# Kernel optimization log

Measured on AMD Instinct MI355X. Metric: run time of the kernel, lower is better.

The kernel has to match this reference:

```python
import jax, jax.numpy as jnp
import numpy as np

B, T, H = 8192, 24, 1024


def setup_inputs() -> dict:
    key = jax.random.key(0)
    ks = jax.random.split(key, 16)
    n = lambda k, shp, s=1.0: (jax.random.normal(k, shp, dtype=jnp.float32) * s)
    return {
        "x": n(ks[0], (B, T, 1)),
        "h1_0": n(ks[1], (B, H), 0.02),
        "c1_0": n(ks[2], (B, H), 0.02),
        "h2_0": n(ks[3], (B, H), 0.02),
        "c2_0": n(ks[4], (B, H), 0.02),
        "W_ih1": n(ks[5], (4 * H, 1), 0.05),
        "W_hh1": n(ks[6], (4 * H, H), 0.02),
        "b_ih1": n(ks[7], (4 * H,), 0.02),
        "b_hh1": n(ks[8], (4 * H,), 0.02),
        "W_ih2": n(ks[9], (4 * H, H), 0.02),
        "W_hh2": n(ks[10], (4 * H, H), 0.02),
        "b_ih2": n(ks[11], (4 * H,), 0.02),
        "b_hh2": n(ks[12], (4 * H,), 0.02),
        "W_out": n(ks[13], (2, H), 0.02),
        "b_out": jnp.array([0.2, -0.2], dtype=jnp.float32),
    }


def _lstm_cell(x_t, h, c, W_ih, W_hh, b_ih, b_hh):
    # PyTorch LSTMCell: gates ordered (i, f, g, o)
    gates = x_t @ W_ih.T + b_ih + h @ W_hh.T + b_hh  # [B, 4H]
    i, f, g, o = jnp.split(gates, 4, axis=-1)
    c_new = jax.nn.sigmoid(f) * c + jax.nn.sigmoid(i) * jnp.tanh(g)
    h_new = jax.nn.sigmoid(o) * jnp.tanh(c_new)
    return h_new, c_new


def reference(x, h1_0, c1_0, h2_0, c2_0,
              W_ih1, W_hh1, b_ih1, b_hh1,
              W_ih2, W_hh2, b_ih2, b_hh2,
              W_out, b_out):
    xs = jnp.transpose(x, (1, 0, 2))  # [T, B, 1]

    def step(carry, x_t):
        h1, c1, h2, c2 = carry
        h1, c1 = _lstm_cell(x_t, h1, c1, W_ih1, W_hh1, b_ih1, b_hh1)
        h2, c2 = _lstm_cell(h1, h2, c2, W_ih2, W_hh2, b_ih2, b_hh2)
        return (h1, c1, h2, c2), None

    (h1, c1, h2, c2), _ = jax.lax.scan(step, (h1_0, c1_0, h2_0, c2_0), xs)
    return h2 @ W_out.T + b_out  # [B, 2]
```

## Files before the change

kernel.cpp:

```cpp
#include <hip/hip_runtime.h>
#include <hip/hip_bf16.h>
#include <stdint.h>

#define B_SZ 8192
#define T_SZ 24
#define H_SZ 1024
#define G4   4096

typedef __attribute__((ext_vector_type(8))) short bf16x8;
typedef __attribute__((ext_vector_type(4))) float f32x4;

#define DSR(dst, base, imm) \
    asm volatile("ds_read_b128 %0, %1 offset:" #imm : "=v"(dst) : "v"(base))

__device__ __forceinline__ int perm_old(int p) {
    int gate = (p >> 4) & 3;
    int unit = ((p >> 6) << 4) | (p & 15);
    return gate * 1024 + unit;
}

__device__ __forceinline__ float fast_sigmoid(float x) {
    return 1.f / (1.f + __expf(-x));
}
__device__ __forceinline__ float fast_tanh(float x) {
    float ax = __builtin_fabsf(x);
    float e  = __expf(2.f * ax);
    float r  = 1.f - 2.f / (e + 1.f);
    return __builtin_copysignf(r, x);
}

__global__ void k_prep_w1(const float* __restrict__ Whh1, __hip_bfloat16* __restrict__ dst) {
    int i = blockIdx.x * blockDim.x + threadIdx.x;
    int p = i >> 10, k = i & 1023;
    dst[i] = __float2bfloat16(Whh1[(size_t)perm_old(p) * 1024 + k]);
}

__global__ void k_prep_w2(const float* __restrict__ Wih2, const float* __restrict__ Whh2,
                          __hip_bfloat16* __restrict__ dst) {
    int i = blockIdx.x * blockDim.x + threadIdx.x;
    int p = i >> 11, k = i & 2047;
    int old = perm_old(p);
    float v = (k < 1024) ? Wih2[(size_t)old * 1024 + k] : Whh2[(size_t)old * 1024 + (k - 1024)];
    dst[i] = __float2bfloat16(v);
}

__global__ void k_prep_vec(const float* __restrict__ bih1, const float* __restrict__ bhh1,
                           const float* __restrict__ bih2, const float* __restrict__ bhh2,
                           const float* __restrict__ Wih1,
                           float* __restrict__ b1p, float* __restrict__ b2p,
                           float* __restrict__ w1p) {
    int p = blockIdx.x * blockDim.x + threadIdx.x;
    if (p >= G4) return;
    int old = perm_old(p);
    b1p[p] = bih1[old] + bhh1[old];
    b2p[p] = bih2[old] + bhh2[old];
    w1p[p] = Wih1[old];
}

__global__ void k_xT(const float* __restrict__ x, float* __restrict__ xT) {
    int i = blockIdx.x * blockDim.x + threadIdx.x;
    if (i >= B_SZ * T_SZ) return;
    int b = i / T_SZ, t = i % T_SZ;
    xT[t * B_SZ + b] = x[i];
}

__global__ void k_init_state(const float* __restrict__ h1_0, const float* __restrict__ c1_0,
                             const float* __restrict__ h2_0, const float* __restrict__ c2_0,
                             __hip_bfloat16* __restrict__ A2_0, __hip_bfloat16* __restrict__ A2_1,
                             float* __restrict__ c1, float* __restrict__ c2) {
    int i = blockIdx.x * blockDim.x + threadIdx.x;
    if (i >= B_SZ * H_SZ) return;
    int b = i >> 10, j = i & 1023;
    A2_1[(size_t)b * 2048 + j]        = __float2bfloat16(h1_0[i]);
    A2_0[(size_t)b * 2048 + 1024 + j] = __float2bfloat16(h2_0[i]);
    c1[i] = c1_0[i];
    c2[i] = c2_0[i];
}

#define BM 256
#define BN 256
#define BK 64

template<int LAYER>
__global__ __launch_bounds__(512, 2)
void k_gemm_cell(const __hip_bfloat16* __restrict__ A, int lda,
                 const __hip_bfloat16* __restrict__ Bw, int ldb, int K,
                 const float* __restrict__ biasp, const float* __restrict__ wih1p,
                 const float* __restrict__ xT, int t,
                 float* __restrict__ c, __hip_bfloat16* __restrict__ hout) {
    __shared__ short As[2][BM][BK];
    __shared__ short Bs[2][BN][BK];
    const int tid  = threadIdx.x;
    const int lane = tid & 63;
    const int wid  = tid >> 6;

    const int bid = blockIdx.x;
    const int xcd = bid & 7;
    const int i   = bid >> 3;
    const int ml  = (i & 7) | ((i >> 5) << 3);
    const int nl  = (i >> 3) & 3;
    const int m0  = ((xcd & 1) * 16 + ml) * BM;
    const int n0  = ((xcd >> 1) * 4 + nl) * BN;

    const int wm = wid >> 2;
    const int wn = wid & 3;
    const int fr = lane & 15;
    const int kg = lane >> 4;

    const __hip_bfloat16* Abase = A  + (size_t)m0 * lda;
    const __hip_bfloat16* Bbase = Bw + (size_t)n0 * ldb;

    f32x4 acc[8][4];
#pragma unroll
    for (int ii = 0; ii < 8; ++ii)
#pragma unroll
        for (int j = 0; j < 4; ++j) acc[ii][j] = (f32x4)0.f;

    auto stage8A = [&](int buf, int lr0, int kcol) {
        int lr = lr0 + (lane >> 3);
        int scol = (((lane & 7) ^ (lr & 7)) << 3);
        const __hip_bfloat16* gp = Abase + (size_t)lr * lda + kcol + scol;
        __builtin_amdgcn_global_load_lds(
            (const __attribute__((address_space(1))) void*)gp,
            (__attribute__((address_space(3))) void*)(&As[buf][lr0][0]), 16, 0, 0);
    };
    auto stage8B = [&](int buf, int lr0, int kcol) {
        int lr = lr0 + (lane >> 3);
        int scol = (((lane & 7) ^ (lr & 7)) << 3);
        const __hip_bfloat16* gp = Bbase + (size_t)lr * ldb + kcol + scol;
        __builtin_amdgcn_global_load_lds(
            (const __attribute__((address_space(1))) void*)gp,
            (__attribute__((address_space(3))) void*)(&Bs[buf][lr0][0]), 16, 0, 0);
    };
    auto stage_u1 = [&](int kt, int buf) {
#pragma unroll
        for (int j = 0; j < 2; ++j) {
            int rr0 = (wid * 2 + j) * 8;
            int lr0 = (rr0 < 64) ? rr0 : rr0 + 64;
            stage8A(buf, lr0, kt * BK);
        }
    };
    auto stage_u2 = [&](int kt, int buf) {
#pragma unroll
        for (int j = 0; j < 2; ++j) {
            int rr0 = (wid * 2 + j) * 8;
            int lr0 = (rr0 < 64) ? rr0 + 64 : rr0 + 128;
            stage8A(buf, lr0, kt * BK);
        }
    };
    auto stage_u3 = [&](int kt, int buf) {
#pragma unroll
        for (int j = 0; j < 2; ++j) {
            int rr0 = (wid * 2 + j) * 8;
            int lr0 = ((rr0 >> 5) << 6) + (rr0 & 31);
            stage8B(buf, lr0, kt * BK);
        }
    };
    auto stage_u4 = [&](int kt, int buf) {
#pragma unroll
        for (int j = 0; j < 2; ++j) {
            int rr0 = (wid * 2 + j) * 8;
            int lr0 = ((rr0 >> 5) << 6) + 32 + (rr0 & 31);
            stage8B(buf, lr0, kt * BK);
        }
    };

    const unsigned asb = (unsigned)(uintptr_t)(__attribute__((address_space(3))) short*)&As[0][0][0];
    const unsigned bsb = (unsigned)(uintptr_t)(__attribute__((address_space(3))) short*)&Bs[0][0][0];
    const unsigned aoffB = (unsigned)((wm * 128 + fr) * 64) * 2;
    const unsigned boffB = (unsigned)((wn * 64 + fr) * 64) * 2;
    const unsigned ck0B  = (unsigned)((kg ^ (fr & 7)) << 3) * 2;
    const unsigned ck1B  = (unsigned)(((4 + kg) ^ (fr & 7)) << 3) * 2;

    const int NK = K >> 6;

    stage_u1(0, 0); stage_u3(0, 0); stage_u4(0, 0); stage_u2(0, 0);
    stage_u1(1, 1); stage_u3(1, 1); stage_u4(1, 1);
    asm volatile("s_waitcnt vmcnt(6)" ::: "memory");
    __builtin_amdgcn_s_barrier();

    bf16x8 a0[4][2], a1[4][2], b0[2][2], b1[2][2];

    for (int kt = 0; kt < NK; ++kt) {
        const int buf = kt & 1;
        const unsigned bo = (unsigned)buf * 32768u;
        const unsigned bA0 = asb + bo + aoffB + ck0B;
        const unsigned bA1 = asb + bo + aoffB + ck1B;
        const unsigned bB0 = bsb + bo + boffB + ck0B;
        const unsigned bB1 = bsb + bo + boffB + ck1B;

        DSR(a0[0][0], bA0, 0);    DSR(a0[0][1], bA1, 0);
        DSR(a0[1][0], bA0, 2048); DSR(a0[1][1], bA1, 2048);
        DSR(a0[2][0], bA0, 4096); DSR(a0[2][1], bA1, 4096);
        DSR(a0[3][0], bA0, 6144); DSR(a0[3][1], bA1, 6144);
        DSR(b0[0][0], bB0, 0);    DSR(b0[0][1], bB1, 0);
        DSR(b0[1][0], bB0, 2048); DSR(b0[1][1], bB1, 2048);
        if (kt + 1 < NK) stage_u2(kt + 1, buf ^ 1);
        asm volatile("s_waitcnt lgkmcnt(8)" ::: "memory");
        __builtin_amdgcn_s_barrier();
        asm volatile("s_waitcnt lgkmcnt(0)" ::: "memory");
        __builtin_amdgcn_sched_barrier(0);
        __builtin_amdgcn_s_setprio(1);
#pragma unroll
        for (int ks = 0; ks < 2; ++ks)
#pragma unroll
            for (int m = 0; m < 4; ++m)
#pragma unroll
                for (int n = 0; n < 2; ++n)
                    acc[m][n] = __builtin_amdgcn_mfma_f32_16x16x32_bf16(a0[m][ks], b0[n][ks], acc[m][n], 0, 0, 0);
        __builtin_amdgcn_s_setprio(0);
        __builtin_amdgcn_s_barrier();

        DSR(b1[0][0], bB0, 4096); DSR(b1[0][1], bB1, 4096);
        DSR(b1[1][0], bB0, 6144); DSR(b1[1][1], bB1, 6144);
        if (kt + 2 < NK) stage_u1(kt + 2, buf);
        __builtin_amdgcn_s_barrier();
        asm volatile("s_waitcnt lgkmcnt(0)" ::: "memory");
        __builtin_amdgcn_sched_barrier(0);
        __builtin_amdgcn_s_setprio(1);
#pragma unroll
        for (int ks = 0; ks < 2; ++ks)
#pragma unroll
            for (int m = 0; m < 4; ++m)
#pragma unroll
                for (int n = 0; n < 2; ++n)
                    acc[m][2 + n] = __builtin_amdgcn_mfma_f32_16x16x32_bf16(a0[m][ks], b1[n][ks], acc[m][2 + n], 0, 0, 0);
        __builtin_amdgcn_s_setprio(0);
        __builtin_amdgcn_s_barrier();

        DSR(a1[0][0], bA0, 8192);  DSR(a1[0][1], bA1, 8192);
        DSR(a1[1][0], bA0, 10240); DSR(a1[1][1], bA1, 10240);
        DSR(a1[2][0], bA0, 12288); DSR(a1[2][1], bA1, 12288);
        DSR(a1[3][0], bA0, 14336); DSR(a1[3][1], bA1, 14336);
        if (kt + 2 < NK) stage_u3(kt + 2, buf);
        __builtin_amdgcn_s_barrier();
        asm volatile("s_waitcnt lgkmcnt(0)" ::: "memory");
        __builtin_amdgcn_sched_barrier(0);
        __builtin_amdgcn_s_setprio(1);
#pragma unroll
        for (int ks = 0; ks < 2; ++ks)
#pragma unroll
            for (int m = 0; m < 4; ++m)
#pragma unroll
                for (int n = 0; n < 2; ++n)
                    acc[4 + m][n] = __builtin_amdgcn_mfma_f32_16x16x32_bf16(a1[m][ks], b0[n][ks], acc[4 + m][n], 0, 0, 0);
        __builtin_amdgcn_s_setprio(0);
        __builtin_amdgcn_s_barrier();

        if (kt + 2 < NK) stage_u4(kt + 2, buf);
        __builtin_amdgcn_s_barrier();
        __builtin_amdgcn_s_setprio(1);
#pragma unroll
        for (int ks = 0; ks < 2; ++ks)
#pragma unroll
            for (int m = 0; m < 4; ++m)
#pragma unroll
                for (int n = 0; n < 2; ++n)
                    acc[4 + m][2 + n] = __builtin_amdgcn_mfma_f32_16x16x32_bf16(a1[m][ks], b1[n][ks], acc[4 + m][2 + n], 0, 0, 0);
        __builtin_amdgcn_s_setprio(0);
        if (kt + 2 < NK)      asm volatile("s_waitcnt vmcnt(6)" ::: "memory");
        else if (kt + 1 < NK) asm volatile("s_waitcnt vmcnt(0)" ::: "memory");
        __builtin_amdgcn_s_barrier();
    }

    float biasv[4], xwv[4];
#pragma unroll
    for (int n = 0; n < 4; ++n) {
        int col = n0 + wn * 64 + n * 16 + fr;
        biasv[n] = biasp[col];
        if (LAYER == 1) xwv[n] = wih1p[col];
    }
    const int u = ((n0 >> 6) + wn) * 16 + fr;

#pragma unroll
    for (int m = 0; m < 8; ++m) {
        int rbase = m0 + wm * 128 + m * 16 + (lane >> 4) * 4;
#pragma unroll
        for (int j = 0; j < 4; ++j) {
            int b = rbase + j;
            float gi = acc[m][0][j] + biasv[0];
            float gf = acc[m][1][j] + biasv[1];
            float gg = acc[m][2][j] + biasv[2];
            float go = acc[m][3][j] + biasv[3];
            if (LAYER == 1) {
                float xv = xT[t * B_SZ + b];
                gi += xv * xwv[0];
                gf += xv * xwv[1];
                gg += xv * xwv[2];
                go += xv * xwv[3];
            }
            float si = fast_sigmoid(gi);
            float sf = fast_sigmoid(gf);
            float so = fast_sigmoid(go);
            float tg = fast_tanh(gg);
            size_t ci = (size_t)b * H_SZ + u;
            float cn = sf * c[ci] + si * tg;
            c[ci] = cn;
            hout[(size_t)b * 2048 + u] = __float2bfloat16(so * fast_tanh(cn));
        }
    }
}

__global__ __launch_bounds__(256)
void k_out(const __hip_bfloat16* __restrict__ h2base, const float* __restrict__ Wout,
           const float* __restrict__ bout, float* __restrict__ out) {
    int gw   = (blockIdx.x * blockDim.x + threadIdx.x) >> 6;
    int lane = threadIdx.x & 63;
    if (gw >= B_SZ) return;
    const __hip_bfloat16* h = h2base + (size_t)gw * 2048;
    float a0 = 0.f, a1 = 0.f;
#pragma unroll
    for (int k = lane; k < 1024; k += 64) {
        float hv = __bfloat162float(h[k]);
        a0 += hv * Wout[k];
        a1 += hv * Wout[1024 + k];
    }
    for (int off = 32; off; off >>= 1) {
        a0 += __shfl_down(a0, off);
        a1 += __shfl_down(a1, off);
    }
    if (lane == 0) {
        out[gw * 2 + 0] = a0 + bout[0];
        out[gw * 2 + 1] = a1 + bout[1];
    }
}

extern "C" void kernel_launch(void* const* d_in, const int* in_sizes, int n_in,
                              void* d_out, int out_size, void* d_ws, size_t ws_size,
                              hipStream_t stream) {
    const float* x    = (const float*)d_in[0];
    const float* h1_0 = (const float*)d_in[1];
    const float* c1_0 = (const float*)d_in[2];
    const float* h2_0 = (const float*)d_in[3];
    const float* c2_0 = (const float*)d_in[4];
    const float* Wih1 = (const float*)d_in[5];
    const float* Whh1 = (const float*)d_in[6];
    const float* bih1 = (const float*)d_in[7];
    const float* bhh1 = (const float*)d_in[8];
    const float* Wih2 = (const float*)d_in[9];
    const float* Whh2 = (const float*)d_in[10];
    const float* bih2 = (const float*)d_in[11];
    const float* bhh2 = (const float*)d_in[12];
    const float* Wout = (const float*)d_in[13];
    const float* bout = (const float*)d_in[14];
    float* out = (float*)d_out;
    (void)in_sizes; (void)n_in; (void)out_size; (void)ws_size;

    uint8_t* ws = (uint8_t*)d_ws;
    size_t off = 0;
    auto alloc = [&](size_t bytes) { void* p = ws + off; off += (bytes + 255) & ~(size_t)255; return p; };
    __hip_bfloat16* A2_0  = (__hip_bfloat16*)alloc((size_t)B_SZ * 2048 * 2);
    __hip_bfloat16* A2_1  = (__hip_bfloat16*)alloc((size_t)B_SZ * 2048 * 2);
    float*          c1    = (float*)alloc((size_t)B_SZ * H_SZ * 4);
    float*          c2    = (float*)alloc((size_t)B_SZ * H_SZ * 4);
    __hip_bfloat16* Whh1p = (__hip_bfloat16*)alloc((size_t)G4 * H_SZ * 2);
    __hip_bfloat16* Wcat2p= (__hip_bfloat16*)alloc((size_t)G4 * 2048 * 2);
    float*          bias1p= (float*)alloc(G4 * 4);
    float*          bias2p= (float*)alloc(G4 * 4);
    float*          wih1p = (float*)alloc(G4 * 4);
    float*          xT    = (float*)alloc((size_t)T_SZ * B_SZ * 4);

    __hip_bfloat16* A2[2] = { A2_0, A2_1 };

    k_prep_w1<<<(G4 * H_SZ + 255) / 256, 256, 0, stream>>>(Whh1, Whh1p);
    k_prep_w2<<<(G4 * 2048 + 255) / 256, 256, 0, stream>>>(Wih2, Whh2, Wcat2p);
    k_prep_vec<<<(G4 + 255) / 256, 256, 0, stream>>>(bih1, bhh1, bih2, bhh2, Wih1,
                                                     bias1p, bias2p, wih1p);
    k_xT<<<(B_SZ * T_SZ + 255) / 256, 256, 0, stream>>>(x, xT);
    k_init_state<<<(B_SZ * H_SZ + 255) / 256, 256, 0, stream>>>(h1_0, c1_0, h2_0, c2_0,
                                                                A2_0, A2_1, c1, c2);

    const int gemm_blocks = (B_SZ / BM) * (G4 / BN);

    for (int t = 0; t < T_SZ; ++t) {
        __hip_bfloat16* Pprev = A2[(t + 1) & 1];
        __hip_bfloat16* Pt    = A2[t & 1];
        k_gemm_cell<1><<<gemm_blocks, 512, 0, stream>>>(
            (const __hip_bfloat16*)Pprev, 2048, Whh1p, 1024, 1024,
            bias1p, wih1p, xT, t, c1, Pt);
        k_gemm_cell<2><<<gemm_blocks, 512, 0, stream>>>(
            (const __hip_bfloat16*)Pt, 2048, Wcat2p, 2048, 2048,
            bias2p, nullptr, nullptr, 0, c2, A2[(t + 1) & 1] + 1024);
    }
    k_out<<<(B_SZ * 64 + 255) / 256, 256, 0, stream>>>(A2_0 + 1024, Wout, bout, out);
}
```

Measured before the change: 5.277 ms.

## Fuse layer-2 step t with layer-1 step t+1 into one kernel

Pulls the GEMM-plus-LSTM-cell body into a device function and adds a templated k_step kernel. Each block runs layer 2 for timestep t, then layer 1 for timestep t+1, since both only need h1_t from the same buffer. This skews the schedule into a wavefront, dropping the launch count from 48 to 25 and removing a kernel boundary and tail per step. The epilogue also loads the cell state c and the x inputs into registers before the activation math, so those global loads overlap. In exchange each block runs longer and register pressure rises, and the ping-pong buffer indexing now carries correctness risk.

```diff
diff --git a/kernel.cpp b/kernel.cpp
--- a/kernel.cpp
+++ b/kernel.cpp
@@ -82,25 +82,14 @@
 #define BK 64
 
 template<int LAYER>
-__global__ __launch_bounds__(512, 2)
-void k_gemm_cell(const __hip_bfloat16* __restrict__ A, int lda,
-                 const __hip_bfloat16* __restrict__ Bw, int ldb, int K,
-                 const float* __restrict__ biasp, const float* __restrict__ wih1p,
-                 const float* __restrict__ xT, int t,
-                 float* __restrict__ c, __hip_bfloat16* __restrict__ hout) {
-    __shared__ short As[2][BM][BK];
-    __shared__ short Bs[2][BN][BK];
-    const int tid  = threadIdx.x;
-    const int lane = tid & 63;
-    const int wid  = tid >> 6;
-
-    const int bid = blockIdx.x;
-    const int xcd = bid & 7;
-    const int i   = bid >> 3;
-    const int ml  = (i & 7) | ((i >> 5) << 3);
-    const int nl  = (i >> 3) & 3;
-    const int m0  = ((xcd & 1) * 16 + ml) * BM;
-    const int n0  = ((xcd >> 1) * 4 + nl) * BN;
+__device__ __forceinline__ void gemm_cell_body(
+    short (&As)[2][BM][BK], short (&Bs)[2][BN][BK],
+    int lane, int wid, int m0, int n0,
+    const __hip_bfloat16* __restrict__ A, int lda,
+    const __hip_bfloat16* __restrict__ Bw, int ldb, int K,
+    const float* __restrict__ biasp, const float* __restrict__ wih1p,
+    const float* __restrict__ xT, int t,
+    float* __restrict__ c, __hip_bfloat16* __restrict__ hout) {
 
     const int wm = wid >> 2;
     const int wn = wid & 3;
@@ -270,35 +259,74 @@
         biasv[n] = biasp[col];
         if (LAYER == 1) xwv[n] = wih1p[col];
     }
-    const int u = ((n0 >> 6) + wn) * 16 + fr;
+    const int u   = ((n0 >> 6) + wn) * 16 + fr;
+    const int rb0 = m0 + wm * 128 + (lane >> 4) * 4;
+
+    float cr[8][4], xv[8][4];
+#pragma unroll
+    for (int m = 0; m < 8; ++m)
+#pragma unroll
+        for (int j = 0; j < 4; ++j) {
+            int b = rb0 + m * 16 + j;
+            cr[m][j] = c[(size_t)b * H_SZ + u];
+            if (LAYER == 1) xv[m][j] = xT[t * B_SZ + b];
+        }
 
 #pragma unroll
     for (int m = 0; m < 8; ++m) {
-        int rbase = m0 + wm * 128 + m * 16 + (lane >> 4) * 4;
 #pragma unroll
         for (int j = 0; j < 4; ++j) {
-            int b = rbase + j;
+            int b = rb0 + m * 16 + j;
             float gi = acc[m][0][j] + biasv[0];
             float gf = acc[m][1][j] + biasv[1];
             float gg = acc[m][2][j] + biasv[2];
             float go = acc[m][3][j] + biasv[3];
             if (LAYER == 1) {
-                float xv = xT[t * B_SZ + b];
-                gi += xv * xwv[0];
-                gf += xv * xwv[1];
-                gg += xv * xwv[2];
-                go += xv * xwv[3];
+                gi += xv[m][j] * xwv[0];
+                gf += xv[m][j] * xwv[1];
+                gg += xv[m][j] * xwv[2];
+                go += xv[m][j] * xwv[3];
             }
             float si = fast_sigmoid(gi);
             float sf = fast_sigmoid(gf);
             float so = fast_sigmoid(go);
             float tg = fast_tanh(gg);
-            size_t ci = (size_t)b * H_SZ + u;
-            float cn = sf * c[ci] + si * tg;
-            c[ci] = cn;
+            float cn = sf * cr[m][j] + si * tg;
+            c[(size_t)b * H_SZ + u] = cn;
             hout[(size_t)b * 2048 + u] = __float2bfloat16(so * fast_tanh(cn));
         }
     }
+}
+
+template<int MODE>
+__global__ __launch_bounds__(512, 2)
+void k_step(const __hip_bfloat16* __restrict__ Pt,
+            const __hip_bfloat16* __restrict__ W2, const float* __restrict__ bias2,
+            float* __restrict__ c2,
+            const __hip_bfloat16* __restrict__ W1, const float* __restrict__ bias1,
+            const float* __restrict__ wih1p, const float* __restrict__ xT, int t_next,
+            float* __restrict__ c1, __hip_bfloat16* __restrict__ Pnext) {
+    __shared__ short As[2][BM][BK];
+    __shared__ short Bs[2][BN][BK];
+    const int lane = threadIdx.x & 63;
+    const int wid  = threadIdx.x >> 6;
+
+    const int bid = blockIdx.x;
+    const int xcd = bid & 7;
+    const int i   = bid >> 3;
+    const int ml  = (i & 7) | ((i >> 5) << 3);
+    const int nl  = (i >> 3) & 3;
+    const int m0  = ((xcd & 1) * 16 + ml) * BM;
+    const int n0  = ((xcd >> 1) * 4 + nl) * BN;
+
+    if (MODE & 1)
+        gemm_cell_body<2>(As, Bs, lane, wid, m0, n0,
+                          Pt, 2048, W2, 2048, 2048,
+                          bias2, nullptr, nullptr, 0, c2, Pnext + 1024);
+    if (MODE & 2)
+        gemm_cell_body<1>(As, Bs, lane, wid, m0, n0,
+                          Pt, 2048, W1, 1024, 1024,
+                          bias1, wih1p, xT, t_next, c1, Pnext);
 }
 
 __global__ __launch_bounds__(256)
@@ -372,15 +400,19 @@
 
     const int gemm_blocks = (B_SZ / BM) * (G4 / BN);
 
-    for (int t = 0; t < T_SZ; ++t) {
-        __hip_bfloat16* Pprev = A2[(t + 1) & 1];
-        __hip_bfloat16* Pt    = A2[t & 1];
-        k_gemm_cell<1><<<gemm_blocks, 512, 0, stream>>>(
-            (const __hip_bfloat16*)Pprev, 2048, Whh1p, 1024, 1024,
-            bias1p, wih1p, xT, t, c1, Pt);
-        k_gemm_cell<2><<<gemm_blocks, 512, 0, stream>>>(
-            (const __hip_bfloat16*)Pt, 2048, Wcat2p, 2048, 2048,
-            bias2p, nullptr, nullptr, 0, c2, A2[(t + 1) & 1] + 1024);
-    }
+    k_step<2><<<gemm_blocks, 512, 0, stream>>>(
+        (const __hip_bfloat16*)A2_1, Wcat2p, bias2p, c2,
+        Whh1p, bias1p, wih1p, xT, 0, c1, A2_0);
+
+    for (int t = 0; t < 23; ++t) {
+        k_step<3><<<gemm_blocks, 512, 0, stream>>>(
+            (const __hip_bfloat16*)A2[t & 1], Wcat2p, bias2p, c2,
+            Whh1p, bias1p, wih1p, xT, t + 1, c1, A2[(t + 1) & 1]);
+    }
+
+    k_step<1><<<gemm_blocks, 512, 0, stream>>>(
+        (const __hip_bfloat16*)A2_1, Wcat2p, bias2p, c2,
+        Whh1p, bias1p, wih1p, xT, 0, c1, A2_0);
+
     k_out<<<(B_SZ * 64 + 255) / 256, 256, 0, stream>>>(A2_0 + 1024, Wout, bout, out);
 }
```

After: 5.749 ms. +8.9%, slower.

## Restructure GEMM main loop to prefetch next tile's LDS fragments across iterations

Applied to the files above, without the earlier changes.

Reorders the four MFMA quadrants in the double-buffered GEMM loop and moves the a0/b0 LDS reads for the next k-tile to the end of the current iteration, with a prologue that preloads the first tile. Global-to-LDS staging is rescheduled so u4/u2 of tile kt+1 and u3/u1 of kt+2 are issued at different points, and the vmcnt/lgkmcnt waits change to match. The aim is to hide LDS read latency behind MFMA work and cut stalls at the barriers. The risk is subtle hazards in buffer reuse and wait counts, plus higher register pressure from keeping fragments live across iterations.

```diff
diff --git a/kernel.cpp b/kernel.cpp
--- a/kernel.cpp
+++ b/kernel.cpp
@@ -174,31 +174,43 @@
 
     const int NK = K >> 6;
 
-    stage_u1(0, 0); stage_u3(0, 0); stage_u4(0, 0); stage_u2(0, 0);
-    stage_u1(1, 1); stage_u3(1, 1); stage_u4(1, 1);
-    asm volatile("s_waitcnt vmcnt(6)" ::: "memory");
+    bf16x8 a0[4][2], a1[4][2], b0[2][2], b1[2][2];
+
+    stage_u1(0, 0); stage_u3(0, 0); stage_u2(0, 0); stage_u4(0, 0);
+    stage_u3(1, 1); stage_u1(1, 1);
+    asm volatile("s_waitcnt vmcnt(4)" ::: "memory");
     __builtin_amdgcn_s_barrier();
-
-    bf16x8 a0[4][2], a1[4][2], b0[2][2], b1[2][2];
+    {
+        const unsigned bA0 = asb + aoffB + ck0B;
+        const unsigned bA1 = asb + aoffB + ck1B;
+        const unsigned bB0 = bsb + boffB + ck0B;
+        const unsigned bB1 = bsb + boffB + ck1B;
+        DSR(b0[0][0], bB0, 0);    DSR(b0[0][1], bB1, 0);
+        DSR(b0[1][0], bB0, 2048); DSR(b0[1][1], bB1, 2048);
+        DSR(a0[0][0], bA0, 0);    DSR(a0[0][1], bA1, 0);
+        DSR(a0[1][0], bA0, 2048); DSR(a0[1][1], bA1, 2048);
+        DSR(a0[2][0], bA0, 4096); DSR(a0[2][1], bA1, 4096);
+        DSR(a0[3][0], bA0, 6144); DSR(a0[3][1], bA1, 6144);
+    }
 
     for (int kt = 0; kt < NK; ++kt) {
         const int buf = kt & 1;
-        const unsigned bo = (unsigned)buf * 32768u;
+        const unsigned bo  = (unsigned)buf * 32768u;
+        const unsigned nbo = bo ^ 32768u;
         const unsigned bA0 = asb + bo + aoffB + ck0B;
         const unsigned bA1 = asb + bo + aoffB + ck1B;
         const unsigned bB0 = bsb + bo + boffB + ck0B;
         const unsigned bB1 = bsb + bo + boffB + ck1B;
-
-        DSR(a0[0][0], bA0, 0);    DSR(a0[0][1], bA1, 0);
-        DSR(a0[1][0], bA0, 2048); DSR(a0[1][1], bA1, 2048);
-        DSR(a0[2][0], bA0, 4096); DSR(a0[2][1], bA1, 4096);
-        DSR(a0[3][0], bA0, 6144); DSR(a0[3][1], bA1, 6144);
-        DSR(b0[0][0], bB0, 0);    DSR(b0[0][1], bB1, 0);
-        DSR(b0[1][0], bB0, 2048); DSR(b0[1][1], bB1, 2048);
-        if (kt + 1 < NK) stage_u2(kt + 1, buf ^ 1);
-        asm volatile("s_waitcnt lgkmcnt(8)" ::: "memory");
-        __builtin_amdgcn_s_barrier();
-        asm volatile("s_waitcnt lgkmcnt(0)" ::: "memory");
+        const unsigned nA0 = asb + nbo + aoffB + ck0B;
+        const unsigned nA1 = asb + nbo + aoffB + ck1B;
+        const unsigned nB0 = bsb + nbo + boffB + ck0B;
+        const unsigned nB1 = bsb + nbo + boffB + ck1B;
+
+        DSR(b1[0][0], bB0, 4096); DSR(b1[0][1], bB1, 4096);
+        DSR(b1[1][0], bB0, 6144); DSR(b1[1][1], bB1, 6144);
+        if (kt + 1 < NK) { stage_u4(kt + 1, buf ^ 1); stage_u2(kt + 1, buf ^ 1); }
+        __builtin_amdgcn_s_barrier();
+        asm volatile("s_waitcnt lgkmcnt(4)" ::: "memory");
         __builtin_amdgcn_sched_barrier(0);
         __builtin_amdgcn_s_setprio(1);
 #pragma unroll
@@ -208,23 +220,6 @@
 #pragma unroll
                 for (int n = 0; n < 2; ++n)
                     acc[m][n] = __builtin_amdgcn_mfma_f32_16x16x32_bf16(a0[m][ks], b0[n][ks], acc[m][n], 0, 0, 0);
-        __builtin_amdgcn_s_setprio(0);
-        __builtin_amdgcn_s_barrier();
-
-        DSR(b1[0][0], bB0, 4096); DSR(b1[0][1], bB1, 4096);
-        DSR(b1[1][0], bB0, 6144); DSR(b1[1][1], bB1, 6144);
-        if (kt + 2 < NK) stage_u1(kt + 2, buf);
-        __builtin_amdgcn_s_barrier();
-        asm volatile("s_waitcnt lgkmcnt(0)" ::: "memory");
-        __builtin_amdgcn_sched_barrier(0);
-        __builtin_amdgcn_s_setprio(1);
-#pragma unroll
-        for (int ks = 0; ks < 2; ++ks)
-#pragma unroll
-            for (int m = 0; m < 4; ++m)
-#pragma unroll
-                for (int n = 0; n < 2; ++n)
-                    acc[m][2 + n] = __builtin_amdgcn_mfma_f32_16x16x32_bf16(a0[m][ks], b1[n][ks], acc[m][2 + n], 0, 0, 0);
         __builtin_amdgcn_s_setprio(0);
         __builtin_amdgcn_s_barrier();
 
@@ -232,7 +227,22 @@
         DSR(a1[1][0], bA0, 10240); DSR(a1[1][1], bA1, 10240);
         DSR(a1[2][0], bA0, 12288); DSR(a1[2][1], bA1, 12288);
         DSR(a1[3][0], bA0, 14336); DSR(a1[3][1], bA1, 14336);
-        if (kt + 2 < NK) stage_u3(kt + 2, buf);
+        __builtin_amdgcn_s_barrier();
+        asm volatile("s_waitcnt lgkmcnt(8)" ::: "memory");
+        __builtin_amdgcn_sched_barrier(0);
+        __builtin_amdgcn_s_setprio(1);
+#pragma unroll
+        for (int ks = 0; ks < 2; ++ks)
+#pragma unroll
+            for (int m = 0; m < 4; ++m)
+#pragma unroll
+                for (int n = 0; n < 2; ++n)
+                    acc[m][2 + n] = __builtin_amdgcn_mfma_f32_16x16x32_bf16(a0[m][ks], b1[n][ks], acc[m][2 + n], 0, 0, 0);
+        __builtin_amdgcn_s_setprio(0);
+        asm volatile("s_waitcnt vmcnt(4)" ::: "memory");
+        __builtin_amdgcn_s_barrier();
+
+        if (kt + 2 < NK) { stage_u3(kt + 2, buf); stage_u1(kt + 2, buf); }
         __builtin_amdgcn_s_barrier();
         asm volatile("s_waitcnt lgkmcnt(0)" ::: "memory");
         __builtin_amdgcn_sched_barrier(0);
@@ -243,23 +253,29 @@
             for (int m = 0; m < 4; ++m)
 #pragma unroll
                 for (int n = 0; n < 2; ++n)
+                    acc[4 + m][2 + n] = __builtin_amdgcn_mfma_f32_16x16x32_bf16(a1[m][ks], b1[n][ks], acc[4 + m][2 + n], 0, 0, 0);
+        __builtin_amdgcn_s_setprio(0);
+        __builtin_amdgcn_s_barrier();
+
+        __builtin_amdgcn_s_setprio(1);
+#pragma unroll
+        for (int ks = 0; ks < 2; ++ks)
+#pragma unroll
+            for (int m = 0; m < 4; ++m)
+#pragma unroll
+                for (int n = 0; n < 2; ++n)
                     acc[4 + m][n] = __builtin_amdgcn_mfma_f32_16x16x32_bf16(a1[m][ks], b0[n][ks], acc[4 + m][n], 0, 0, 0);
         __builtin_amdgcn_s_setprio(0);
-        __builtin_amdgcn_s_barrier();
-
-        if (kt + 2 < NK) stage_u4(kt + 2, buf);
-        __builtin_amdgcn_s_barrier();
-        __builtin_amdgcn_s_setprio(1);
-#pragma unroll
-        for (int ks = 0; ks < 2; ++ks)
-#pragma unroll
-            for (int m = 0; m < 4; ++m)
-#pragma unroll
-                for (int n = 0; n < 2; ++n)
-                    acc[4 + m][2 + n] = __builtin_amdgcn_mfma_f32_16x16x32_bf16(a1[m][ks], b1[n][ks], acc[4 + m][2 + n], 0, 0, 0);
-        __builtin_amdgcn_s_setprio(0);
-        if (kt + 2 < NK)      asm volatile("s_waitcnt vmcnt(6)" ::: "memory");
-        else if (kt + 1 < NK) asm volatile("s_waitcnt vmcnt(0)" ::: "memory");
+        __builtin_amdgcn_sched_barrier(0);
+        if (kt + 1 < NK) {
+            DSR(b0[0][0], nB0, 0);    DSR(b0[0][1], nB1, 0);
+            DSR(b0[1][0], nB0, 2048); DSR(b0[1][1], nB1, 2048);
+            DSR(a0[0][0], nA0, 0);    DSR(a0[0][1], nA1, 0);
+            DSR(a0[1][0], nA0, 2048); DSR(a0[1][1], nA1, 2048);
+            DSR(a0[2][0], nA0, 4096); DSR(a0[2][1], nA1, 4096);
+            DSR(a0[3][0], nA0, 6144); DSR(a0[3][1], nA1, 6144);
+        }
+        asm volatile("s_waitcnt vmcnt(4)" ::: "memory");
         __builtin_amdgcn_s_barrier();
     }
 
```

Result: no change. 5.211 ms (-1.3%).
